# Kernel optimization log

Hardware: AMD Instinct MI355X
Metric: run time of the kernel (lower is better)

## Reference

```python
import jax, jax.numpy as jnp
import numpy as np

N_EMBD = 1024
N_HEAD = 16
HEAD_SIZE = 64


def setup_inputs() -> dict:
    key = jax.random.key(0)
    ks = jax.random.split(key, 6)
    B, T, C, H, D = 2, 2048, N_EMBD, N_HEAD, HEAD_SIZE
    s = 1.0 / np.sqrt(C)
    x = jax.random.normal(ks[0], (B, T, C), dtype=jnp.float32)
    Wq = jax.random.normal(ks[1], (H, C, D), dtype=jnp.float32) * s
    Wk = jax.random.normal(ks[2], (H, C, D), dtype=jnp.float32) * s
    Wv = jax.random.normal(ks[3], (H, C, D), dtype=jnp.float32) * s
    Wo = jax.random.normal(ks[4], (H * D, C), dtype=jnp.float32) * (1.0 / np.sqrt(H * D))
    bo = jax.random.normal(ks[5], (C,), dtype=jnp.float32) * 0.01
    return {"x": x, "Wq": Wq, "Wk": Wk, "Wv": Wv, "Wo": Wo, "bo": bo}


def reference(x, Wq, Wk, Wv, Wo, bo):
    B, T, C = x.shape
    H, _, D = Wq.shape
    # Per-head projections, batched across heads: [B,H,T,D]
    q = jnp.einsum('btc,hcd->bhtd', x, Wq)
    k = jnp.einsum('btc,hcd->bhtd', x, Wk)
    v = jnp.einsum('btc,hcd->bhtd', x, Wv)
    # NOTE: original scales by sqrt(C) = sqrt(n_embd), not sqrt(head_size)
    scale = 1.0 / jnp.sqrt(jnp.float32(C))
    att = jnp.einsum('bhtd,bhsd->bhts', q, k) * scale  # [B,H,T,T]
    causal = jnp.tril(jnp.ones((T, T), dtype=bool))
    att = jnp.where(causal, att, -jnp.inf)
    att = jax.nn.softmax(att, axis=-1)
    # dropout omitted (eval mode / deterministic reference)
    out = jnp.einsum('bhts,bhsd->bhtd', att, v)  # [B,H,T,D]
    out = out.transpose(0, 2, 1, 3).reshape(B, T, H * D)
    return out @ Wo + bo
```

## Files before the change

### kernel.cpp

```cpp
#include <hip/hip_runtime.h>
#include <hip/hip_bf16.h>


typedef __hip_bfloat16 bf16;
typedef __bf16 v8bf __attribute__((ext_vector_type(8)));
typedef float  v4f  __attribute__((ext_vector_type(4)));
typedef unsigned long long u64;
typedef unsigned int u32;

#define MFMA16(a, b, c) __builtin_amdgcn_mfma_f32_16x16x32_bf16((a), (b), (c), 0, 0, 0)

__device__ __forceinline__ bf16 f2b(float x) { return __float2bfloat16(x); }
__device__ __forceinline__ __bf16 f2braw(float x) {
  bf16 t = __float2bfloat16(x);
  return *reinterpret_cast<__bf16*>(&t);
}
__device__ __forceinline__ unsigned short f2bu(float x) {
  bf16 t = __float2bfloat16(x);
  return *reinterpret_cast<unsigned short*>(&t);
}

__device__ __forceinline__ void load16_lds(const bf16* gptr, const bf16* lptr) {
  __builtin_amdgcn_global_load_lds(
      (const __attribute__((address_space(1))) u32*)gptr,
      (__attribute__((address_space(3))) u32*)lptr, 16, 0, 0);
}

__global__ __launch_bounds__(256) void prep_kernel(
    const float* __restrict__ x,
    const float* __restrict__ Wq, const float* __restrict__ Wk,
    const float* __restrict__ Wv, const float* __restrict__ Wo,
    bf16* __restrict__ xb, bf16* __restrict__ wt, bf16* __restrict__ wot)
{
  __shared__ float Lt[32][33];
  const int bid = blockIdx.x, tid = threadIdx.x;

  if (bid < 2048) {
    size_t i = ((size_t)bid * 256 + tid) * 8;
    float4 f0 = *(const float4*)(x + i);
    float4 f1 = *(const float4*)(x + i + 4);
    v8bf v;
    v[0] = f2braw(f0.x); v[1] = f2braw(f0.y); v[2] = f2braw(f0.z); v[3] = f2braw(f0.w);
    v[4] = f2braw(f1.x); v[5] = f2braw(f1.y); v[6] = f2braw(f1.z); v[7] = f2braw(f1.w);
    *(v8bf*)(xb + i) = v;
    return;
  }
  const int tx = tid & 31, ty = tid >> 5;
  if (bid < 5120) {
    const int idx = bid - 2048;
    const int z = idx >> 6, rem = idx & 63;
    const int p = z >> 4, h = z & 15;
    const float* ib = ((p == 0) ? Wq : (p == 1) ? Wk : Wv) + (size_t)h * 65536;
    bf16* ob = wt + (size_t)z * 65536;
    const int j0 = (rem & 1) * 32, i0 = (rem >> 1) * 32;
    #pragma unroll
    for (int r = 0; r < 4; ++r)
      Lt[ty + 8 * r][tx] = ib[(size_t)(i0 + ty + 8 * r) * 64 + j0 + tx];
    __syncthreads();
    #pragma unroll
    for (int r = 0; r < 4; ++r)
      ob[(size_t)(j0 + ty + 8 * r) * 1024 + i0 + tx] = f2b(Lt[tx][ty + 8 * r]);
  } else {
    const int idx = bid - 5120;
    const int j0 = (idx & 31) * 32, i0 = (idx >> 5) * 32;
    #pragma unroll
    for (int r = 0; r < 4; ++r)
      Lt[ty + 8 * r][tx] = Wo[(size_t)(i0 + ty + 8 * r) * 1024 + j0 + tx];
    __syncthreads();
    #pragma unroll
    for (int r = 0; r < 4; ++r)
      wot[(size_t)(j0 + ty + 8 * r) * 1024 + i0 + tx] = f2b(Lt[tx][ty + 8 * r]);
  }
}

__global__ __launch_bounds__(256) void qkv_gemm_kernel(
    const bf16* __restrict__ xb, const bf16* __restrict__ wt,
    bf16* __restrict__ qkv)
{
  __shared__ __align__(16) bf16 Ash[2][128][32];
  __shared__ __align__(16) bf16 Bsh[2][128][32];

  const int mt = blockIdx.x, nt = blockIdx.y;
  const int tid = threadIdx.x, w = tid >> 6, lane = tid & 63;
  const int ln = lane & 15, quad = lane >> 4;
  const int wm = w >> 1, wn = w & 1;
  const int m0 = mt * 128, n0 = nt * 128;

  const v4f vzero = {0.f, 0.f, 0.f, 0.f};
  v4f acc[4][4];
  #pragma unroll
  for (int mf = 0; mf < 4; ++mf)
    #pragma unroll
    for (int nf = 0; nf < 4; ++nf) acc[mf][nf] = vzero;

  const int srow = lane >> 2;
  const int sseg = ((lane & 3) ^ ((lane >> 3) & 3)) * 8;
  const bf16* ga = xb + (size_t)(m0 + 32 * w + srow) * 1024 + sseg;
  const bf16* gb = wt + (size_t)(n0 + 32 * w + srow) * 1024 + sseg;

  const int fseg = (quad ^ ((ln >> 1) & 3)) * 8;

  load16_lds(ga,             &Ash[0][32 * w][0]);
  load16_lds(ga + 16 * 1024, &Ash[0][32 * w + 16][0]);
  load16_lds(gb,             &Bsh[0][32 * w][0]);
  load16_lds(gb + 16 * 1024, &Bsh[0][32 * w + 16][0]);
  ga += 32; gb += 32;

  int kt = 0;
  #define GTILE(BUF)                                                     \
  {                                                                      \
    __syncthreads();                                  \
    v8bf af[4], bfv[4];                                                  \
    _Pragma("unroll")                                                    \
    for (int mf = 0; mf < 4; ++mf)                                       \
      af[mf] = *(const v8bf*)&Ash[BUF][wm * 64 + mf * 16 + ln][fseg];    \
    _Pragma("unroll")                                                    \
    for (int nf = 0; nf < 4; ++nf)                                       \
      bfv[nf] = *(const v8bf*)&Bsh[BUF][wn * 64 + nf * 16 + ln][fseg];   \
    if (kt < 31) {                            \
      load16_lds(ga,             &Ash[BUF ^ 1][32 * w][0]);              \
      load16_lds(ga + 16 * 1024, &Ash[BUF ^ 1][32 * w + 16][0]);         \
      load16_lds(gb,             &Bsh[BUF ^ 1][32 * w][0]);              \
      load16_lds(gb + 16 * 1024, &Bsh[BUF ^ 1][32 * w + 16][0]);         \
      ga += 32; gb += 32;                                                \
    }                                                                    \
    _Pragma("unroll")                                                    \
    for (int mf = 0; mf < 4; ++mf)                                       \
      _Pragma("unroll")                                                  \
      for (int nf = 0; nf < 4; ++nf)                                     \
        acc[mf][nf] = MFMA16(af[mf], bfv[nf], acc[mf][nf]);              \
    ++kt;                                                                \
  }

  #pragma unroll 1
  for (int it = 0; it < 16; ++it) {
    GTILE(0)
    GTILE(1)
  }
  #undef GTILE

  const int jcol0 = n0 + wn * 64;
  const int p = jcol0 >> 10;
  const int h = (jcol0 >> 6) & 15;
  const float scale = (p == 0) ? 0.0450841149f : 1.0f;

  if (p < 2) {
    bf16* base = qkv + (size_t)p * 4194304 + (size_t)h * 262144;
    #pragma unroll
    for (int mf = 0; mf < 4; ++mf)
      #pragma unroll
      for (int nf = 0; nf < 4; ++nf) {
        int d = nf * 16 + ln;
        #pragma unroll
        for (int r = 0; r < 4; ++r) {
          int m = m0 + wm * 64 + mf * 16 + quad * 4 + r;
          base[(size_t)m * 64 + d] = f2b(acc[mf][nf][r] * scale);
        }
      }
  } else {
    bf16* vb = qkv + (size_t)2 * 4194304 + (size_t)h * 262144;
    #pragma unroll
    for (int mf = 0; mf < 4; ++mf) {
      int mrow = m0 + wm * 64 + mf * 16 + quad * 4;
      int bi = mrow >> 11, t0 = mrow & 2047;
      #pragma unroll
      for (int nf = 0; nf < 4; ++nf) {
        int d = nf * 16 + ln;
        u64 pk = (u64)f2bu(acc[mf][nf][0]) |
                 ((u64)f2bu(acc[mf][nf][1]) << 16) |
                 ((u64)f2bu(acc[mf][nf][2]) << 32) |
                 ((u64)f2bu(acc[mf][nf][3]) << 48);
        *(u64*)(vb + (size_t)bi * 131072 + (size_t)d * 2048 + t0) = pk;
      }
    }
  }
}

__global__ __launch_bounds__(256, 4) void attn_kernel(
    const bf16* __restrict__ qkv, bf16* __restrict__ att)
{
  union ShU {
    struct { bf16 K[2][64][64]; bf16 V[2][64][64]; } t;
    struct { float O[2][64][36]; float L[2][36]; } c;
  };
  __shared__ __align__(16) ShU sh;

  const int fid = blockIdx.x;
  const int j = fid >> 5;
  const int jr = j & 7, jq = j >> 3;
  const int mt = (jq == 0) ? (31 - jr) : (jq == 1) ? (8 + jr)
               : (jq == 2) ? (23 - jr) : jr;
  const int grp = fid & 31;
  const int b = grp >> 4, h = grp & 15;

  const int tid = threadIdx.x, w = tid >> 6, lane = tid & 63;
  const int ln = lane & 15, quad = lane >> 4;
  const int qh = w & 1, kh = w >> 1;

  const bf16* qbase  = qkv + (size_t)h * 262144 + (size_t)b * 131072;
  const bf16* kbase  = qbase + 4194304;
  const bf16* vtbase = qbase + 8388608;

  const int l8 = lane & 7, r8 = lane >> 3;
  const int slot = l8 ^ r8;
  const int p0 = w * 16 + r8, p1 = p0 + 8;
  const int kp0 = (p0 & 32) | ((p0 & 12) << 1) | ((p0 & 16) >> 2) | (p0 & 3);
  const int kp1 = (p1 & 32) | ((p1 & 12) << 1) | ((p1 & 16) >> 2) | (p1 & 3);
  const bf16* gkp0 = kbase + kp0 * 64 + slot * 8;
  const bf16* gkp1 = kbase + kp1 * 64 + slot * 8;
  const bf16* gvp0 = vtbase + p0 * 2048 + slot * 8;
  const bf16* gvp1 = gvp0 + 8 * 2048;

  const int sw = ln & 7;
  const int cc0 = ((quad    ) ^ sw) * 8;
  const int cc1 = ((quad + 4) ^ sw) * 8;
  const int cck = kh ? cc1 : cc0;
  const int krow0 = (kh * 32 + ln) * 64;
  const int ka0 = krow0 + cc0, ka1 = krow0 + cc1;
  const int voff = ln * 64 + cck;

  v8bf vone;
  {
    unsigned short u = 0x3F80;
    __bf16 e = *reinterpret_cast<__bf16*>(&u);
    #pragma unroll
    for (int jj = 0; jj < 8; ++jj) vone[jj] = e;
  }
  const v4f vzero = {0.f, 0.f, 0.f, 0.f};
  const float NEG = -30000.0f;

  #define STAGE2(BUF) {                                          \
    load16_lds(gkp0, &sh.t.K[BUF][w * 16][0]);                   \
    load16_lds(gkp1, &sh.t.K[BUF][w * 16 + 8][0]);               \
    load16_lds(gvp0, &sh.t.V[BUF][w * 16][0]);                   \
    load16_lds(gvp1, &sh.t.V[BUF][w * 16 + 8][0]);               \
    gkp0 += 4096; gkp1 += 4096; gvp0 += 64; gvp1 += 64; }

  const int row0 = mt * 64;
  const int qrow = row0 + qh * 32;

  v8bf aq[2][2];
  #pragma unroll
  for (int mc = 0; mc < 2; ++mc)
    #pragma unroll
    for (int ks = 0; ks < 2; ++ks)
      aq[mc][ks] = *(const v8bf*)(qbase +
          (size_t)(qrow + mc * 16 + ln) * 64 + ks * 32 + quad * 8);

  v4f o[2][4], lacc[2];
  #pragma unroll
  for (int mc = 0; mc < 2; ++mc) {
    lacc[mc] = vzero;
    #pragma unroll
    for (int dt = 0; dt < 4; ++dt) o[mc][dt] = vzero;
  }

  const int kb_end = mt;
  int kb = 0;
  STAGE2(0)

  #define TILE(BUF)                                                        \
  {                                                                        \
    __syncthreads();                                    \
    const bf16* krB = &sh.t.K[BUF][0][0];                                  \
    const bf16* vrB = &sh.t.V[BUF][0][0];                                  \
    v8bf kf[2][2], vf[4];                                                  \
    kf[0][0] = *(const v8bf*)(krB + ka0);                                  \
    kf[1][0] = *(const v8bf*)(krB + ka1);                                  \
    kf[0][1] = *(const v8bf*)(krB + ka0 + 1024);                           \
    kf[1][1] = *(const v8bf*)(krB + ka1 + 1024);                           \
    vf[0] = *(const v8bf*)(vrB + voff);                                    \
    vf[1] = *(const v8bf*)(vrB + voff + 1024);                             \
    vf[2] = *(const v8bf*)(vrB + voff + 2048);                             \
    vf[3] = *(const v8bf*)(vrB + voff + 3072);                             \
    if (kb < kb_end) STAGE2(BUF ^ 1)                                       \
    _Pragma("unroll")                                                      \
    for (int mc = 0; mc < 2; ++mc) {                                       \
      __builtin_amdgcn_s_setprio(1);                                       \
      v4f s[2];                                                            \
      s[0] = vzero; s[1] = vzero;                                          \
      _Pragma("unroll")                                                    \
      for (int ks = 0; ks < 2; ++ks) {                                     \
        s[0] = MFMA16(kf[ks][0], aq[mc][ks], s[0]);                        \
        s[1] = MFMA16(kf[ks][1], aq[mc][ks], s[1]);                        \
      }                                                                    \
      __builtin_amdgcn_s_setprio(0);                                       \
      const int qg = qrow + mc * 16 + ln;                                  \
      if (kb == kb_end) {                      \
        _Pragma("unroll")                                                  \
        for (int nfl = 0; nfl < 2; ++nfl) {                                \
          const int kc = kb * 64 + kh * 32 + quad * 8 + nfl * 4;           \
          _Pragma("unroll")                                                \
          for (int r = 0; r < 4; ++r)                                      \
            if (kc + r > qg) s[nfl][r] = NEG;                              \
        }                                                                  \
      }                                                                    \
      float ex[2][4];                                                      \
      _Pragma("unroll")                                                    \
      for (int nfl = 0; nfl < 2; ++nfl)                                    \
        _Pragma("unroll")                                                  \
        for (int r = 0; r < 4; ++r)                                        \
          ex[nfl][r] = exp2f(s[nfl][r]);                                   \
      union { u32 uw[4]; v8bf v; } pu;                                     \
      _Pragma("unroll")                                                    \
      for (int nfl = 0; nfl < 2; ++nfl)                                    \
        _Pragma("unroll")                                                  \
        for (int wi = 0; wi < 2; ++wi)                                     \
          asm("v_cvt_pk_bf16_f32 %0, %1, %2"                               \
              : "=v"(pu.uw[nfl * 2 + wi])                                  \
              : "v"(ex[nfl][2 * wi]), "v"(ex[nfl][2 * wi + 1]));           \
      __builtin_amdgcn_s_setprio(1);                                       \
      lacc[mc] = MFMA16(pu.v, vone, lacc[mc]);                             \
      _Pragma("unroll")                                                    \
      for (int dt = 0; dt < 4; ++dt)                                       \
        o[mc][dt] = MFMA16(pu.v, vf[dt], o[mc][dt]);                       \
      __builtin_amdgcn_s_setprio(0);                                       \
    }                                                                      \
  }

  while (true) {
    TILE(0)
    if (kb >= kb_end) break;
    ++kb;
    TILE(1)
    if (kb >= kb_end) break;
    ++kb;
  }
  #undef TILE
  #undef STAGE2

  __syncthreads();
  if (kh == 1) {
    #pragma unroll
    for (int mc = 0; mc < 2; ++mc) {
      #pragma unroll
      for (int dt = 0; dt < 4; ++dt)
        *(v4f*)&sh.c.O[qh][dt * 16 + ln][mc * 16 + quad * 4] = o[mc][dt];
      if (ln == 0)
        *(v4f*)&sh.c.L[qh][mc * 16 + quad * 4] = lacc[mc];
    }
  }
  __syncthreads();
  if (kh == 0) {
    #pragma unroll
    for (int mc = 0; mc < 2; ++mc) {
      v4f pl = *(const v4f*)&sh.c.L[qh][mc * 16 + quad * 4];
      v4f inv;
      #pragma unroll
      for (int r = 0; r < 4; ++r) inv[r] = 1.0f / (lacc[mc][r] + pl[r]);
      #pragma unroll
      for (int dt = 0; dt < 4; ++dt) {
        v4f po = *(const v4f*)&sh.c.O[qh][dt * 16 + ln][mc * 16 + quad * 4];
        #pragma unroll
        for (int r = 0; r < 4; ++r) {
          int m = b * 2048 + qrow + mc * 16 + quad * 4 + r;
          att[(size_t)m * 1024 + h * 64 + dt * 16 + ln] =
              f2b((o[mc][dt][r] + po[r]) * inv[r]);
        }
      }
    }
  }
}

__global__ __launch_bounds__(256) void out_gemm_kernel(
    const bf16* __restrict__ att, const bf16* __restrict__ wot,
    const float* __restrict__ bo, float* __restrict__ out)
{
  __shared__ __align__(16) bf16 Ash[2][128][32];
  __shared__ __align__(16) bf16 Bsh[2][64][32];

  const int mt = blockIdx.x, nt = blockIdx.y;
  const int tid = threadIdx.x, w = tid >> 6, lane = tid & 63;
  const int ln = lane & 15, quad = lane >> 4;
  const int wm = w >> 1, wn = w & 1;
  const int m0 = mt * 128, n0 = nt * 64;

  const v4f vzero = {0.f, 0.f, 0.f, 0.f};
  v4f acc[4][2];
  #pragma unroll
  for (int mf = 0; mf < 4; ++mf)
    #pragma unroll
    for (int nf = 0; nf < 2; ++nf) acc[mf][nf] = vzero;

  const int srow = lane >> 2;
  const int sseg = ((lane & 3) ^ ((lane >> 3) & 3)) * 8;
  const bf16* ga = att + (size_t)(m0 + 32 * w + srow) * 1024 + sseg;
  const bf16* gb = wot + (size_t)(n0 + 16 * w + srow) * 1024 + sseg;

  const int fseg = (quad ^ ((ln >> 1) & 3)) * 8;

  load16_lds(ga,             &Ash[0][32 * w][0]);
  load16_lds(ga + 16 * 1024, &Ash[0][32 * w + 16][0]);
  load16_lds(gb,             &Bsh[0][16 * w][0]);
  ga += 32; gb += 32;

  int kt = 0;
  #define OTILE(BUF)                                                     \
  {                                                                      \
    __syncthreads();                                                     \
    v8bf af[4], bfv[2];                                                  \
    _Pragma("unroll")                                                    \
    for (int mf = 0; mf < 4; ++mf)                                       \
      af[mf] = *(const v8bf*)&Ash[BUF][wm * 64 + mf * 16 + ln][fseg];    \
    _Pragma("unroll")                                                    \
    for (int nf = 0; nf < 2; ++nf)                                       \
      bfv[nf] = *(const v8bf*)&Bsh[BUF][wn * 32 + nf * 16 + ln][fseg];   \
    if (kt < 31) {                                                       \
      load16_lds(ga,             &Ash[BUF ^ 1][32 * w][0]);              \
      load16_lds(ga + 16 * 1024, &Ash[BUF ^ 1][32 * w + 16][0]);         \
      load16_lds(gb,             &Bsh[BUF ^ 1][16 * w][0]);              \
      ga += 32; gb += 32;                                                \
    }                                                                    \
    _Pragma("unroll")                                                    \
    for (int mf = 0; mf < 4; ++mf)                                       \
      _Pragma("unroll")                                                  \
      for (int nf = 0; nf < 2; ++nf)                                     \
        acc[mf][nf] = MFMA16(af[mf], bfv[nf], acc[mf][nf]);              \
    ++kt;                                                                \
  }

  #pragma unroll 1
  for (int it = 0; it < 16; ++it) {
    OTILE(0)
    OTILE(1)
  }
  #undef OTILE

  #pragma unroll
  for (int nf = 0; nf < 2; ++nf) {
    int j = n0 + wn * 32 + nf * 16 + ln;
    float bias = bo[j];
    #pragma unroll
    for (int mf = 0; mf < 4; ++mf)
      #pragma unroll
      for (int r = 0; r < 4; ++r) {
        int m = m0 + wm * 64 + mf * 16 + quad * 4 + r;
        out[(size_t)m * 1024 + j] = acc[mf][nf][r] + bias;
      }
  }
}

extern "C" void kernel_launch(void* const* d_in, const int* in_sizes, int n_in,
                              void* d_out, int out_size, void* d_ws, size_t ws_size,
                              hipStream_t stream) {
  const float* x  = (const float*)d_in[0];
  const float* Wq = (const float*)d_in[1];
  const float* Wk = (const float*)d_in[2];
  const float* Wv = (const float*)d_in[3];
  const float* Wo = (const float*)d_in[4];
  const float* bo = (const float*)d_in[5];
  float* out = (float*)d_out;

  bf16* xb  = (bf16*)d_ws;
  bf16* wt  = xb + 4194304;
  bf16* wot = xb + 7340032;
  bf16* qkv = xb + 8388608;
  bf16* att = xb + 20971520;

  prep_kernel<<<6144, 256, 0, stream>>>(x, Wq, Wk, Wv, Wo, xb, wt, wot);
  qkv_gemm_kernel<<<dim3(32, 24), 256, 0, stream>>>(xb, wt, qkv);
  attn_kernel<<<1024, 256, 0, stream>>>(qkv, att);
  out_gemm_kernel<<<dim3(32, 16), 256, 0, stream>>>(att, wot, bo, out);
}
```

Before: 167.2 us.

## Retile QKV GEMM to 256x192 blocks with triple-buffered LDS pipeline

Changes the QKV projection GEMM from 128x128 tiles with 256 threads to 256x192 tiles with 512 threads (8 waves, each 64x96). The grid drops from 768 to 256 blocks, which roughly matches the CU count. Global-to-LDS loads become a three-stage ring with explicit vmcnt waits and raw barriers, and MFMA priority is raised during compute to hide load latency better. The larger accumulator footprint raises register pressure, and the tail B rows are clamped, so some loads are redundant.

```diff
diff --git a/kernel.cpp b/kernel.cpp
--- a/kernel.cpp
+++ b/kernel.cpp
@@ -73,99 +73,102 @@
   }
 }
 
-__global__ __launch_bounds__(256) void qkv_gemm_kernel(
+__global__ __launch_bounds__(512, 2) void qkv_gemm_kernel(
     const bf16* __restrict__ xb, const bf16* __restrict__ wt,
     bf16* __restrict__ qkv)
 {
-  __shared__ __align__(16) bf16 Ash[2][128][32];
-  __shared__ __align__(16) bf16 Bsh[2][128][32];
+  __shared__ __align__(16) bf16 Ash[3][256][32];
+  __shared__ __align__(16) bf16 Bsh[3][256][32];
 
   const int mt = blockIdx.x, nt = blockIdx.y;
-  const int tid = threadIdx.x, w = tid >> 6, lane = tid & 63;
+  const int tid = threadIdx.x, wid = tid >> 6, lane = tid & 63;
   const int ln = lane & 15, quad = lane >> 4;
-  const int wm = w >> 1, wn = w & 1;
-  const int m0 = mt * 128, n0 = nt * 128;
+  const int wm = wid >> 1, wn = wid & 1;
+  const int m0 = mt * 256, n0 = nt * 192;
 
   const v4f vzero = {0.f, 0.f, 0.f, 0.f};
-  v4f acc[4][4];
+  v4f acc[4][6];
   #pragma unroll
   for (int mf = 0; mf < 4; ++mf)
     #pragma unroll
-    for (int nf = 0; nf < 4; ++nf) acc[mf][nf] = vzero;
+    for (int nf = 0; nf < 6; ++nf) acc[mf][nf] = vzero;
 
   const int srow = lane >> 2;
   const int sseg = ((lane & 3) ^ ((lane >> 3) & 3)) * 8;
-  const bf16* ga = xb + (size_t)(m0 + 32 * w + srow) * 1024 + sseg;
-  const bf16* gb = wt + (size_t)(n0 + 32 * w + srow) * 1024 + sseg;
+  const int arow = wid * 32 + srow;
+  const int br0 = wid * 32 + srow,  brow0 = (br0 < 192) ? br0 : 191;
+  const int br1 = wid * 32 + 16 + srow, brow1 = (br1 < 192) ? br1 : 191;
+  const bf16* ga  = xb + (size_t)(m0 + arow) * 1024 + sseg;
+  const bf16* gb0 = wt + (size_t)(n0 + brow0) * 1024 + sseg;
+  const bf16* gb1 = wt + (size_t)(n0 + brow1) * 1024 + sseg;
 
   const int fseg = (quad ^ ((ln >> 1) & 3)) * 8;
 
-  load16_lds(ga,             &Ash[0][32 * w][0]);
-  load16_lds(ga + 16 * 1024, &Ash[0][32 * w + 16][0]);
-  load16_lds(gb,             &Bsh[0][32 * w][0]);
-  load16_lds(gb + 16 * 1024, &Bsh[0][32 * w + 16][0]);
-  ga += 32; gb += 32;
-
-  int kt = 0;
-  #define GTILE(BUF)                                                     \
-  {                                                                      \
-    __syncthreads();                                  \
-    v8bf af[4], bfv[4];                                                  \
-    _Pragma("unroll")                                                    \
-    for (int mf = 0; mf < 4; ++mf)                                       \
-      af[mf] = *(const v8bf*)&Ash[BUF][wm * 64 + mf * 16 + ln][fseg];    \
-    _Pragma("unroll")                                                    \
-    for (int nf = 0; nf < 4; ++nf)                                       \
-      bfv[nf] = *(const v8bf*)&Bsh[BUF][wn * 64 + nf * 16 + ln][fseg];   \
-    if (kt < 31) {                            \
-      load16_lds(ga,             &Ash[BUF ^ 1][32 * w][0]);              \
-      load16_lds(ga + 16 * 1024, &Ash[BUF ^ 1][32 * w + 16][0]);         \
-      load16_lds(gb,             &Bsh[BUF ^ 1][32 * w][0]);              \
-      load16_lds(gb + 16 * 1024, &Bsh[BUF ^ 1][32 * w + 16][0]);         \
-      ga += 32; gb += 32;                                                \
-    }                                                                    \
-    _Pragma("unroll")                                                    \
-    for (int mf = 0; mf < 4; ++mf)                                       \
-      _Pragma("unroll")                                                  \
-      for (int nf = 0; nf < 4; ++nf)                                     \
-        acc[mf][nf] = MFMA16(af[mf], bfv[nf], acc[mf][nf]);              \
-    ++kt;                                                                \
+  #define QSTAGE(BUF) {                                          \
+    load16_lds(ga,              &Ash[BUF][wid * 32][0]);         \
+    load16_lds(ga + 16 * 1024,  &Ash[BUF][wid * 32 + 16][0]);    \
+    load16_lds(gb0,             &Bsh[BUF][wid * 32][0]);         \
+    load16_lds(gb1,             &Bsh[BUF][wid * 32 + 16][0]);    \
+    ga += 32; gb0 += 32; gb1 += 32; }
+
+  QSTAGE(0)
+  QSTAGE(1)
+
+  #define QSTEP(BUF, VM, DOSTAGE)                                          \
+  {                                                                        \
+    asm volatile("s_waitcnt vmcnt(" #VM ") lgkmcnt(0)" ::: "memory");      \
+    __builtin_amdgcn_s_barrier();                                          \
+    __builtin_amdgcn_sched_barrier(0);                                     \
+    v8bf af[4], bfv[6];                                                    \
+    _Pragma("unroll")                                                      \
+    for (int mf = 0; mf < 4; ++mf)                                         \
+      af[mf] = *(const v8bf*)&Ash[BUF][wm * 64 + mf * 16 + ln][fseg];      \
+    _Pragma("unroll")                                                      \
+    for (int nf = 0; nf < 6; ++nf)                                         \
+      bfv[nf] = *(const v8bf*)&Bsh[BUF][wn * 96 + nf * 16 + ln][fseg];     \
+    if (DOSTAGE) QSTAGE((BUF + 2) % 3)                                     \
+    __builtin_amdgcn_s_setprio(1);                                         \
+    _Pragma("unroll")                                                      \
+    for (int mf = 0; mf < 4; ++mf)                                         \
+      _Pragma("unroll")                                                    \
+      for (int nf = 0; nf < 6; ++nf)                                       \
+        acc[mf][nf] = MFMA16(af[mf], bfv[nf], acc[mf][nf]);                \
+    __builtin_amdgcn_s_setprio(0);                                         \
   }
 
   #pragma unroll 1
-  for (int it = 0; it < 16; ++it) {
-    GTILE(0)
-    GTILE(1)
-  }
-  #undef GTILE
-
-  const int jcol0 = n0 + wn * 64;
-  const int p = jcol0 >> 10;
-  const int h = (jcol0 >> 6) & 15;
-  const float scale = (p == 0) ? 0.0450841149f : 1.0f;
-
-  if (p < 2) {
-    bf16* base = qkv + (size_t)p * 4194304 + (size_t)h * 262144;
-    #pragma unroll
-    for (int mf = 0; mf < 4; ++mf)
-      #pragma unroll
-      for (int nf = 0; nf < 4; ++nf) {
-        int d = nf * 16 + ln;
+  for (int it = 0; it < 10; ++it) {
+    QSTEP(0, 4, 1)
+    QSTEP(1, 4, 1)
+    QSTEP(2, 4, 1)
+  }
+  QSTEP(0, 4, 0)
+  QSTEP(1, 0, 0)
+  #undef QSTEP
+  #undef QSTAGE
+
+  #pragma unroll
+  for (int nf = 0; nf < 6; ++nf) {
+    const int j = n0 + wn * 96 + nf * 16 + ln;
+    const int p = j >> 10;
+    const int h = (j >> 6) & 15;
+    const int d = j & 63;
+    if (p < 2) {
+      const float scale = (p == 0) ? 0.0450841149f : 1.0f;
+      bf16* base = qkv + (size_t)p * 4194304 + (size_t)h * 262144;
+      #pragma unroll
+      for (int mf = 0; mf < 4; ++mf)
         #pragma unroll
         for (int r = 0; r < 4; ++r) {
           int m = m0 + wm * 64 + mf * 16 + quad * 4 + r;
           base[(size_t)m * 64 + d] = f2b(acc[mf][nf][r] * scale);
         }
-      }
-  } else {
-    bf16* vb = qkv + (size_t)2 * 4194304 + (size_t)h * 262144;
-    #pragma unroll
-    for (int mf = 0; mf < 4; ++mf) {
-      int mrow = m0 + wm * 64 + mf * 16 + quad * 4;
-      int bi = mrow >> 11, t0 = mrow & 2047;
-      #pragma unroll
-      for (int nf = 0; nf < 4; ++nf) {
-        int d = nf * 16 + ln;
+    } else {
+      bf16* vb = qkv + (size_t)2 * 4194304 + (size_t)h * 262144;
+      #pragma unroll
+      for (int mf = 0; mf < 4; ++mf) {
+        int mrow = m0 + wm * 64 + mf * 16 + quad * 4;
+        int bi = mrow >> 11, t0 = mrow & 2047;
         u64 pk = (u64)f2bu(acc[mf][nf][0]) |
                  ((u64)f2bu(acc[mf][nf][1]) << 16) |
                  ((u64)f2bu(acc[mf][nf][2]) << 32) |
@@ -458,7 +461,7 @@
   bf16* att = xb + 20971520;
 
   prep_kernel<<<6144, 256, 0, stream>>>(x, Wq, Wk, Wv, Wo, xb, wt, wot);
-  qkv_gemm_kernel<<<dim3(32, 24), 256, 0, stream>>>(xb, wt, qkv);
+  qkv_gemm_kernel<<<dim3(16, 16), 512, 0, stream>>>(xb, wt, qkv);
   attn_kernel<<<1024, 256, 0, stream>>>(qkv, att);
   out_gemm_kernel<<<dim3(32, 16), 256, 0, stream>>>(att, wot, bo, out);
 }
```

After: 165.5 us. About the same (-1.0%).
